# Kernel tuning notes

Measured on AMD Instinct MI355X. Metric: run time of the kernel, lower is better.

Reference implementation:

```python
import jax, jax.numpy as jnp
import numpy as np

NEG_INF = -9e15
LEAKY_SLOPE = 0.2  # init alpha
N, IN_DIM, OUT_DIM = 8192, 512, 256


def setup_inputs() -> dict:
    key = jax.random.key(0)
    k1, k2, k3, k4, k5 = jax.random.split(key, 5)
    h = jax.random.normal(k1, (N, IN_DIM), dtype=jnp.float32)
    adj = jax.random.randint(k2, (N, N), 0, 2, dtype=jnp.int32)
    W = jax.random.normal(k3, (IN_DIM, OUT_DIM), dtype=jnp.float32) * 0.06
    a_left = jax.random.normal(k4, (OUT_DIM, 1), dtype=jnp.float32) * 0.1
    a_right = jax.random.normal(k5, (OUT_DIM, 1), dtype=jnp.float32) * 0.1
    return {"h": h, "adj": adj, "W": W, "a_left": a_left, "a_right": a_right}


def reference(h, adj, W, a_left, a_right):
    Wh = h @ W                                  # [N, out_dim]
    Wh1 = Wh @ a_left                           # [N, 1]
    Wh2 = Wh @ a_right                          # [N, 1]
    e = Wh1 + Wh2.T                             # [N, N] broadcast additive scores
    e = jnp.where(e > 0, e, LEAKY_SLOPE * e)    # LeakyReLU
    e = jnp.where(adj > 0, e, NEG_INF)          # adjacency mask
    attention = jax.nn.softmax(e, axis=1)       # row-wise softmax (dropout=0, eval)
    h_out = attention @ Wh                      # [N, out_dim]
    return jax.nn.elu(h_out)                    # activation=True
```

## Files before the change

kernel.cpp:

```cpp
#include <hip/hip_runtime.h>
#include <hip/hip_bf16.h>
#include <cstdint>
#include <cstddef>

typedef float  f32x4  __attribute__((ext_vector_type(4)));
typedef __bf16 bf16x8 __attribute__((ext_vector_type(8)));

#define LOG2E 1.4426950408889634f

static constexpr int GN   = 8192;
static constexpr int GIN  = 512;
static constexpr int GOUT = 256;

static __device__ __forceinline__ void gload_lds16(const void* g, void* lds){
  typedef uint32_t __attribute__((address_space(1)))* gp_t;
  typedef uint32_t __attribute__((address_space(3)))* lp_t;
  __builtin_amdgcn_global_load_lds((gp_t)(uintptr_t)g,
                                   (lp_t)(uint32_t)(uintptr_t)lds, 16, 0, 0);
}

__global__ void k_wa(const float* __restrict__ W, const float* __restrict__ al,
                     const float* __restrict__ ar, float* __restrict__ wal,
                     float* __restrict__ war){
  int k = blockIdx.x;
  int lane = threadIdx.x;
  float4 wv = ((const float4*)(W + (size_t)k*GOUT))[lane];
  float4 av = ((const float4*)al)[lane];
  float4 bv = ((const float4*)ar)[lane];
  float sl = wv.x*av.x + wv.y*av.y + wv.z*av.z + wv.w*av.w;
  float sr = wv.x*bv.x + wv.y*bv.y + wv.z*bv.z + wv.w*bv.w;
  #pragma unroll
  for(int o=32;o;o>>=1){ sl += __shfl_down(sl,o,64); sr += __shfl_down(sr,o,64); }
  if(lane==0){ wal[k] = sl*LOG2E; war[k] = sr*LOG2E; }
}

__global__ void k_h2b(const float* __restrict__ h, __bf16* __restrict__ hb){
  size_t i = ((size_t)blockIdx.x*256 + threadIdx.x)*8;
  float4 v0 = *(const float4*)(h+i);
  float4 v1 = *(const float4*)(h+i+4);
  bf16x8 o;
  o[0]=(__bf16)v0.x; o[1]=(__bf16)v0.y; o[2]=(__bf16)v0.z; o[3]=(__bf16)v0.w;
  o[4]=(__bf16)v1.x; o[5]=(__bf16)v1.y; o[6]=(__bf16)v1.z; o[7]=(__bf16)v1.w;
  *(bf16x8*)(hb+i) = o;
}

__global__ void k_wt(const float* __restrict__ W, __bf16* __restrict__ WT){
  int idx = blockIdx.x*256 + threadIdx.x;
  int k = idx >> 8, c = idx & 255;
  WT[(size_t)c*GIN + k] = (__bf16)W[idx];
}

__global__ void k_wh12(const float* __restrict__ h, const float* __restrict__ wal,
                       const float* __restrict__ war, float* __restrict__ Wh1,
                       float* __restrict__ Wh2){
  int row = blockIdx.x*4 + (threadIdx.x>>6);
  int lane = threadIdx.x & 63;
  const float4* hp = (const float4*)(h + (size_t)row*GIN);
  const float4* lp = (const float4*)wal;
  const float4* rp = (const float4*)war;
  float sl = 0.f, sr = 0.f;
  #pragma unroll
  for(int t=0;t<2;t++){
    float4 v = hp[lane*2+t];
    float4 a = lp[lane*2+t];
    float4 b = rp[lane*2+t];
    sl += v.x*a.x + v.y*a.y + v.z*a.z + v.w*a.w;
    sr += v.x*b.x + v.y*b.y + v.z*b.z + v.w*b.w;
  }
  #pragma unroll
  for(int o=32;o;o>>=1){ sl += __shfl_down(sl,o,64); sr += __shfl_down(sr,o,64); }
  if(lane==0){ Wh1[row]=sl; Wh2[row]=sr; }
}

__global__ __launch_bounds__(256,1) void k_gemmT(const __bf16* __restrict__ WT,
                                                 const __bf16* __restrict__ hb,
                                                 __bf16* __restrict__ WhbT){
  __shared__ __attribute__((aligned(16))) __bf16 As[2][64*64];
  __shared__ __attribute__((aligned(16))) __bf16 Bs[2][128*64];
  const int tid = threadIdx.x, lane = tid & 63, w = tid >> 6;
  const int mb = blockIdx.x >> 6, nb = blockIdx.x & 63;
  const int m0 = mb*64, n0 = nb*128;

  f32x4 acc[8];
  #pragma unroll
  for(int t=0;t<8;t++) acc[t] = (f32x4){0.f,0.f,0.f,0.f};

  const int lr = lane>>3;
  const int bs_sw = ((lane&7)*16) ^ (lr<<4);

  auto stage = [&](int it, int buf){
    const int k0b = it*128;
    #pragma unroll
    for(int s=0;s<6;s++){
      int u = w + s*4;
      const char* src; char* dst;
      if(u < 8){
        int r8 = u*8;
        src = (const char*)(WT + (size_t)(m0 + r8 + lr)*GIN);
        dst = (char*)&As[buf][0] + r8*128;
      } else {
        int r8 = (u-8)*8;
        src = (const char*)(hb + (size_t)(n0 + r8 + lr)*GIN);
        dst = (char*)&Bs[buf][0] + r8*128;
      }
      gload_lds16(src + k0b + bs_sw, dst);
    }
  };

  auto kstep = [&](int kk, int buf){
    const int ko = kk*64 + (lane>>4)*16;
    const int am = 16*w + (lane&15);
    bf16x8 af = *(const bf16x8*)((const char*)&As[buf][0] + am*128 + (ko ^ ((am&7)<<4)));
    #pragma unroll
    for(int t=0;t<8;t++){
      int n = 16*t + (lane&15);
      bf16x8 bf = *(const bf16x8*)((const char*)&Bs[buf][0] + n*128 + (ko ^ ((n&7)<<4)));
      acc[t] = __builtin_amdgcn_mfma_f32_16x16x32_bf16(af, bf, acc[t], 0, 0, 0);
    }
  };

  stage(0,0);
  asm volatile("s_waitcnt vmcnt(0)" ::: "memory");
  __builtin_amdgcn_s_barrier();
  for(int it=0; it<8; it++){
    int buf = it & 1;
    if(it < 7) stage(it+1, buf^1);
    kstep(0, buf);
    kstep(1, buf);
    asm volatile("s_waitcnt vmcnt(0)" ::: "memory");
    __builtin_amdgcn_s_barrier();
  }

  const int mrow = m0 + 16*w + 4*(lane>>4);
  const int nc0  = n0 + (lane&15);
  #pragma unroll
  for(int t=0;t<8;t++){
    #pragma unroll
    for(int r=0;r<4;r++){
      WhbT[(size_t)(mrow + r)*GN + nc0 + 16*t] = (__bf16)acc[t][r];
    }
  }
}

__global__ __launch_bounds__(256,2) void k_attn(const int* __restrict__ adj,
                                                const __bf16* __restrict__ WhbT,
                                                const float* __restrict__ Wh1s,
                                                const float* __restrict__ Wh2s,
                                                float* __restrict__ accPV,
                                                float* __restrict__ accS){
  __shared__ __attribute__((aligned(16))) __bf16 Vs[2][256*64];
  const int tid = threadIdx.x, lane = tid & 63, w = tid >> 6;
  const int rg = blockIdx.x >> 3, chunk = blockIdx.x & 7;
  const int r0 = rg * 128;
  const int j0 = chunk * 1024;

  f32x4 acc0[16], acc1[16];
  #pragma unroll
  for(int t=0;t<16;t++){ acc0[t] = (f32x4){0.f,0.f,0.f,0.f}; acc1[t] = (f32x4){0.f,0.f,0.f,0.f}; }
  f32x4 accs0 = (f32x4){0.f,0.f,0.f,0.f};
  f32x4 accs1 = (f32x4){0.f,0.f,0.f,0.f};

  bf16x8 ones;
  #pragma unroll
  for(int j=0;j<8;j++) ones[j] = (__bf16)1.0f;

  const int kg = lane >> 4;
  const int myrow0 = r0 + 16*w + (lane & 15);
  const int myrow1 = myrow0 + 64;
  const float wh1_0 = Wh1s[myrow0];
  const float wh1_1 = Wh1s[myrow1];
  const int*   adjrow0 = adj  + (size_t)myrow0*GN + j0 + kg*8;
  const int*   adjrow1 = adj  + (size_t)myrow1*GN + j0 + kg*8;
  const float* wh2p    = Wh2s + j0 + kg*8;

  const int lr = lane>>3;
  const int bs_sw = ((lane&7)*16) ^ (lr<<4);

  auto stage = [&](int it, int buf){
    const int colb = (j0 + it*64)*2;
    #pragma unroll
    for(int s=0;s<8;s++){
      int u = w + s*4;
      int r8 = u*8;
      const char* src = (const char*)WhbT + (size_t)(r8 + lr)*(GN*2) + colb + bs_sw;
      gload_lds16(src, (char*)&Vs[buf][0] + r8*128);
    }
  };

  auto mkpa = [&](float wh1, int4 a0, int4 a1, float4 w0, float4 w1) -> bf16x8 {
    bf16x8 pa;
    float y, p;
    y = wh1 + w0.x; y = fmaxf(y, 0.2f*y); p = exp2f(y); pa[0] = (__bf16)(a0.x ? p : 0.f);
    y = wh1 + w0.y; y = fmaxf(y, 0.2f*y); p = exp2f(y); pa[1] = (__bf16)(a0.y ? p : 0.f);
    y = wh1 + w0.z; y = fmaxf(y, 0.2f*y); p = exp2f(y); pa[2] = (__bf16)(a0.z ? p : 0.f);
    y = wh1 + w0.w; y = fmaxf(y, 0.2f*y); p = exp2f(y); pa[3] = (__bf16)(a0.w ? p : 0.f);
    y = wh1 + w1.x; y = fmaxf(y, 0.2f*y); p = exp2f(y); pa[4] = (__bf16)(a1.x ? p : 0.f);
    y = wh1 + w1.y; y = fmaxf(y, 0.2f*y); p = exp2f(y); pa[5] = (__bf16)(a1.y ? p : 0.f);
    y = wh1 + w1.z; y = fmaxf(y, 0.2f*y); p = exp2f(y); pa[6] = (__bf16)(a1.z ? p : 0.f);
    y = wh1 + w1.w; y = fmaxf(y, 0.2f*y); p = exp2f(y); pa[7] = (__bf16)(a1.w ? p : 0.f);
    return pa;
  };

  auto kstep = [&](int it, int kk, int buf){
    const int off = it*64 + kk*32;
    const int* ap0 = adjrow0 + off;
    const int* ap1 = adjrow1 + off;
    int4 a00 = *(const int4*)ap0;  int4 a01 = *(const int4*)(ap0 + 4);
    int4 a10 = *(const int4*)ap1;  int4 a11 = *(const int4*)(ap1 + 4);
    const float* wp = wh2p + off;
    float4 w0 = *(const float4*)wp;
    float4 w1 = *(const float4*)(wp + 4);
    bf16x8 pa0 = mkpa(wh1_0, a00, a01, w0, w1);
    bf16x8 pa1 = mkpa(wh1_1, a10, a11, w0, w1);
    const int ko = kk*64 + kg*16;
    #pragma unroll
    for(int t=0;t<16;t++){
      int n = 16*t + (lane&15);
      bf16x8 bv = *(const bf16x8*)((const char*)&Vs[buf][0] + n*128 + (ko ^ ((n&7)<<4)));
      acc0[t] = __builtin_amdgcn_mfma_f32_16x16x32_bf16(pa0, bv, acc0[t], 0, 0, 0);
      acc1[t] = __builtin_amdgcn_mfma_f32_16x16x32_bf16(pa1, bv, acc1[t], 0, 0, 0);
    }
    accs0 = __builtin_amdgcn_mfma_f32_16x16x32_bf16(pa0, ones, accs0, 0, 0, 0);
    accs1 = __builtin_amdgcn_mfma_f32_16x16x32_bf16(pa1, ones, accs1, 0, 0, 0);
  };

  stage(0, 0);
  asm volatile("s_waitcnt vmcnt(0)" ::: "memory");
  __builtin_amdgcn_s_barrier();
  for(int it=0; it<16; it++){
    int buf = it & 1;
    if(it < 15) stage(it+1, buf^1);
    kstep(it, 0, buf);
    kstep(it, 1, buf);
    asm volatile("s_waitcnt vmcnt(0)" ::: "memory");
    __builtin_amdgcn_s_barrier();
  }

  const int orow0 = r0 + 16*w + 4*kg;
  const int orow1 = orow0 + 64;
  const int ocol  = lane & 15;
  #pragma unroll
  for(int t=0;t<16;t++){
    #pragma unroll
    for(int r=0;r<4;r++){
      atomicAdd(accPV + (size_t)(orow0 + r)*GOUT + ocol + 16*t, acc0[t][r]);
      atomicAdd(accPV + (size_t)(orow1 + r)*GOUT + ocol + 16*t, acc1[t][r]);
    }
  }
  if(ocol == 0){
    #pragma unroll
    for(int r=0;r<4;r++){
      atomicAdd(accS + orow0 + r, accs0[r]);
      atomicAdd(accS + orow1 + r, accs1[r]);
    }
  }
}

static __device__ __forceinline__ float elu1(float x){
  return x > 0.f ? x : (exp2f(x*LOG2E) - 1.f);
}
__global__ void k_norm(const float* __restrict__ accPV, const float* __restrict__ accS,
                       float* __restrict__ out){
  size_t i = ((size_t)blockIdx.x*256 + threadIdx.x)*4;
  int row = (int)(i >> 8);
  float inv = 1.0f / accS[row];
  float4 v = *(const float4*)(accPV + i);
  float4 o;
  o.x = elu1(v.x*inv); o.y = elu1(v.y*inv); o.z = elu1(v.z*inv); o.w = elu1(v.w*inv);
  *(float4*)(out + i) = o;
}

extern "C" void kernel_launch(void* const* d_in, const int* in_sizes, int n_in,
                              void* d_out, int out_size, void* d_ws, size_t ws_size,
                              hipStream_t stream){
  const float* h  = (const float*)d_in[0];
  const int*   adj= (const int*)  d_in[1];
  const float* W  = (const float*)d_in[2];
  const float* al = (const float*)d_in[3];
  const float* ar = (const float*)d_in[4];
  float* out = (float*)d_out;

  char* ws = (char*)d_ws;
  float*  accPV = (float*) (ws);
  float*  accS  = (float*) (ws + 8388608);
  __bf16* hb    = (__bf16*)(ws + 8421376);
  __bf16* WT    = (__bf16*)(ws + 16809984);
  __bf16* WhbT  = (__bf16*)(ws + 17072128);
  float*  wal   = (float*) (ws + 21266432);
  float*  war   = (float*) (ws + 21268480);
  float*  Wh1   = (float*) (ws + 21270528);
  float*  Wh2   = (float*) (ws + 21303296);
  if(ws_size < 21336064) return;

  hipMemsetAsync(accPV, 0, 8388608 + 32768, stream);

  k_wa  <<<512, 64, 0, stream>>>(W, al, ar, wal, war);
  k_h2b <<<2048, 256, 0, stream>>>(h, hb);
  k_wt  <<<512, 256, 0, stream>>>(W, WT);
  k_wh12<<<2048, 256, 0, stream>>>(h, wal, war, Wh1, Wh2);
  k_gemmT<<<256, 256, 0, stream>>>(WT, hb, WhbT);
  k_attn<<<512, 256, 0, stream>>>(adj, WhbT, Wh1, Wh2, accPV, accS);
  k_norm<<<2048, 256, 0, stream>>>(accPV, accS, out);
}
```

Before: 154.5 us.

## Fuse h prep kernels, ballot-pack adjacency masks, replace atomics with partial-sum reduce

```diff
diff --git a/kernel.cpp b/kernel.cpp
--- a/kernel.cpp
+++ b/kernel.cpp
@@ -34,42 +34,32 @@
   if(lane==0){ wal[k] = sl*LOG2E; war[k] = sr*LOG2E; }
 }
 
-__global__ void k_h2b(const float* __restrict__ h, __bf16* __restrict__ hb){
-  size_t i = ((size_t)blockIdx.x*256 + threadIdx.x)*8;
-  float4 v0 = *(const float4*)(h+i);
-  float4 v1 = *(const float4*)(h+i+4);
+__global__ void k_prep_h(const float* __restrict__ h, const float* __restrict__ wal,
+                         const float* __restrict__ war, __bf16* __restrict__ hb,
+                         float* __restrict__ Wh1, float* __restrict__ Wh2){
+  int row = blockIdx.x*4 + (threadIdx.x>>6);
+  int lane = threadIdx.x & 63;
+  const float4* hp = (const float4*)(h + (size_t)row*GIN);
+  float4 v0 = hp[lane*2], v1 = hp[lane*2+1];
   bf16x8 o;
   o[0]=(__bf16)v0.x; o[1]=(__bf16)v0.y; o[2]=(__bf16)v0.z; o[3]=(__bf16)v0.w;
   o[4]=(__bf16)v1.x; o[5]=(__bf16)v1.y; o[6]=(__bf16)v1.z; o[7]=(__bf16)v1.w;
-  *(bf16x8*)(hb+i) = o;
+  *(bf16x8*)(hb + (size_t)row*GIN + lane*8) = o;
+  float4 a0 = ((const float4*)wal)[lane*2], a1 = ((const float4*)wal)[lane*2+1];
+  float4 b0 = ((const float4*)war)[lane*2], b1 = ((const float4*)war)[lane*2+1];
+  float sl = v0.x*a0.x+v0.y*a0.y+v0.z*a0.z+v0.w*a0.w
+           + v1.x*a1.x+v1.y*a1.y+v1.z*a1.z+v1.w*a1.w;
+  float sr = v0.x*b0.x+v0.y*b0.y+v0.z*b0.z+v0.w*b0.w
+           + v1.x*b1.x+v1.y*b1.y+v1.z*b1.z+v1.w*b1.w;
+  #pragma unroll
+  for(int of=32;of;of>>=1){ sl += __shfl_down(sl,of,64); sr += __shfl_down(sr,of,64); }
+  if(lane==0){ Wh1[row]=sl; Wh2[row]=sr; }
 }
 
 __global__ void k_wt(const float* __restrict__ W, __bf16* __restrict__ WT){
   int idx = blockIdx.x*256 + threadIdx.x;
   int k = idx >> 8, c = idx & 255;
   WT[(size_t)c*GIN + k] = (__bf16)W[idx];
-}
-
-__global__ void k_wh12(const float* __restrict__ h, const float* __restrict__ wal,
-                       const float* __restrict__ war, float* __restrict__ Wh1,
-                       float* __restrict__ Wh2){
-  int row = blockIdx.x*4 + (threadIdx.x>>6);
-  int lane = threadIdx.x & 63;
-  const float4* hp = (const float4*)(h + (size_t)row*GIN);
-  const float4* lp = (const float4*)wal;
-  const float4* rp = (const float4*)war;
-  float sl = 0.f, sr = 0.f;
-  #pragma unroll
-  for(int t=0;t<2;t++){
-    float4 v = hp[lane*2+t];
-    float4 a = lp[lane*2+t];
-    float4 b = rp[lane*2+t];
-    sl += v.x*a.x + v.y*a.y + v.z*a.z + v.w*a.w;
-    sr += v.x*b.x + v.y*b.y + v.z*b.z + v.w*b.w;
-  }
-  #pragma unroll
-  for(int o=32;o;o>>=1){ sl += __shfl_down(sl,o,64); sr += __shfl_down(sr,o,64); }
-  if(lane==0){ Wh1[row]=sl; Wh2[row]=sr; }
 }
 
 __global__ __launch_bounds__(256,1) void k_gemmT(const __bf16* __restrict__ WT,
@@ -142,12 +132,13 @@
   }
 }
 
+template<bool PART>
 __global__ __launch_bounds__(256,2) void k_attn(const int* __restrict__ adj,
                                                 const __bf16* __restrict__ WhbT,
                                                 const float* __restrict__ Wh1s,
                                                 const float* __restrict__ Wh2s,
-                                                float* __restrict__ accPV,
-                                                float* __restrict__ accS){
+                                                float* __restrict__ pv_out,
+                                                float* __restrict__ s_out){
   __shared__ __attribute__((aligned(16))) __bf16 Vs[2][256*64];
   const int tid = threadIdx.x, lane = tid & 63, w = tid >> 6;
   const int rg = blockIdx.x >> 3, chunk = blockIdx.x & 7;
@@ -164,14 +155,15 @@
   #pragma unroll
   for(int j=0;j<8;j++) ones[j] = (__bf16)1.0f;
 
-  const int kg = lane >> 4;
+  const int kg  = lane >> 4;
+  const int kg8 = kg << 3;
   const int myrow0 = r0 + 16*w + (lane & 15);
-  const int myrow1 = myrow0 + 64;
   const float wh1_0 = Wh1s[myrow0];
-  const float wh1_1 = Wh1s[myrow1];
-  const int*   adjrow0 = adj  + (size_t)myrow0*GN + j0 + kg*8;
-  const int*   adjrow1 = adj  + (size_t)myrow1*GN + j0 + kg*8;
-  const float* wh2p    = Wh2s + j0 + kg*8;
+  const float wh1_1 = Wh1s[myrow0 + 64];
+  const float* wh2p = Wh2s + j0 + kg8;
+
+  const size_t arow0 = (size_t)(r0 + 16*w) * GN + j0;
+  const size_t arow1 = arow0 + (size_t)64 * GN;
 
   const int lr = lane>>3;
   const int bs_sw = ((lane&7)*16) ^ (lr<<4);
@@ -187,31 +179,53 @@
     }
   };
 
-  auto mkpa = [&](float wh1, int4 a0, int4 a1, float4 w0, float4 w1) -> bf16x8 {
+  int a0p[16], a1p[16];
+  auto adj_load = [&](int tt){
+    const int co = tt*64 + lane;
+    #pragma unroll
+    for(int r=0;r<16;r++) a0p[r] = adj[arow0 + (size_t)r*GN + co];
+    #pragma unroll
+    for(int r=0;r<16;r++) a1p[r] = adj[arow1 + (size_t)r*GN + co];
+  };
+  auto adj_pack = [&](uint64_t& m0, uint64_t& m1){
+    uint64_t n0 = 0, n1 = 0;
+    #pragma unroll
+    for(int r=0;r<16;r++){
+      uint64_t b = __ballot(a0p[r] != 0);
+      if((lane&15)==r) n0 = b;
+    }
+    #pragma unroll
+    for(int r=0;r<16;r++){
+      uint64_t b = __ballot(a1p[r] != 0);
+      if((lane&15)==r) n1 = b;
+    }
+    m0 = n0; m1 = n1;
+  };
+
+  auto mkpa = [&](float wh1, unsigned m8, float4 w0, float4 w1) -> bf16x8 {
     bf16x8 pa;
     float y, p;
-    y = wh1 + w0.x; y = fmaxf(y, 0.2f*y); p = exp2f(y); pa[0] = (__bf16)(a0.x ? p : 0.f);
-    y = wh1 + w0.y; y = fmaxf(y, 0.2f*y); p = exp2f(y); pa[1] = (__bf16)(a0.y ? p : 0.f);
-    y = wh1 + w0.z; y = fmaxf(y, 0.2f*y); p = exp2f(y); pa[2] = (__bf16)(a0.z ? p : 0.f);
-    y = wh1 + w0.w; y = fmaxf(y, 0.2f*y); p = exp2f(y); pa[3] = (__bf16)(a0.w ? p : 0.f);
-    y = wh1 + w1.x; y = fmaxf(y, 0.2f*y); p = exp2f(y); pa[4] = (__bf16)(a1.x ? p : 0.f);
-    y = wh1 + w1.y; y = fmaxf(y, 0.2f*y); p = exp2f(y); pa[5] = (__bf16)(a1.y ? p : 0.f);
-    y = wh1 + w1.z; y = fmaxf(y, 0.2f*y); p = exp2f(y); pa[6] = (__bf16)(a1.z ? p : 0.f);
-    y = wh1 + w1.w; y = fmaxf(y, 0.2f*y); p = exp2f(y); pa[7] = (__bf16)(a1.w ? p : 0.f);
+    y = wh1 + w0.x; y = fmaxf(y, 0.2f*y); p = exp2f(y); pa[0] = (__bf16)((m8    )&1 ? p : 0.f);
+    y = wh1 + w0.y; y = fmaxf(y, 0.2f*y); p = exp2f(y); pa[1] = (__bf16)((m8>>1)&1 ? p : 0.f);
+    y = wh1 + w0.z; y = fmaxf(y, 0.2f*y); p = exp2f(y); pa[2] = (__bf16)((m8>>2)&1 ? p : 0.f);
+    y = wh1 + w0.w; y = fmaxf(y, 0.2f*y); p = exp2f(y); pa[3] = (__bf16)((m8>>3)&1 ? p : 0.f);
+    y = wh1 + w1.x; y = fmaxf(y, 0.2f*y); p = exp2f(y); pa[4] = (__bf16)((m8>>4)&1 ? p : 0.f);
+    y = wh1 + w1.y; y = fmaxf(y, 0.2f*y); p = exp2f(y); pa[5] = (__bf16)((m8>>5)&1 ? p : 0.f);
+    y = wh1 + w1.z; y = fmaxf(y, 0.2f*y); p = exp2f(y); pa[6] = (__bf16)((m8>>6)&1 ? p : 0.f);
+    y = wh1 + w1.w; y = fmaxf(y, 0.2f*y); p = exp2f(y); pa[7] = (__bf16)((m8>>7)&1 ? p : 0.f);
     return pa;
   };
 
+  uint64_t mk0, mk1;
+
   auto kstep = [&](int it, int kk, int buf){
-    const int off = it*64 + kk*32;
-    const int* ap0 = adjrow0 + off;
-    const int* ap1 = adjrow1 + off;
-    int4 a00 = *(const int4*)ap0;  int4 a01 = *(const int4*)(ap0 + 4);
-    int4 a10 = *(const int4*)ap1;  int4 a11 = *(const int4*)(ap1 + 4);
-    const float* wp = wh2p + off;
+    const float* wp = wh2p + it*64 + kk*32;
     float4 w0 = *(const float4*)wp;
     float4 w1 = *(const float4*)(wp + 4);
-    bf16x8 pa0 = mkpa(wh1_0, a00, a01, w0, w1);
-    bf16x8 pa1 = mkpa(wh1_1, a10, a11, w0, w1);
+    unsigned m8_0 = (unsigned)((mk0 >> (kk*32 + kg8)) & 0xffULL);
+    unsigned m8_1 = (unsigned)((mk1 >> (kk*32 + kg8)) & 0xffULL);
+    bf16x8 pa0 = mkpa(wh1_0, m8_0, w0, w1);
+    bf16x8 pa1 = mkpa(wh1_1, m8_1, w0, w1);
     const int ko = kk*64 + kg*16;
     #pragma unroll
     for(int t=0;t<16;t++){
@@ -225,33 +239,56 @@
   };
 
   stage(0, 0);
+  adj_load(0);
+  adj_pack(mk0, mk1);
   asm volatile("s_waitcnt vmcnt(0)" ::: "memory");
   __builtin_amdgcn_s_barrier();
+
   for(int it=0; it<16; it++){
     int buf = it & 1;
-    if(it < 15) stage(it+1, buf^1);
+    if(it < 15){
+      stage(it+1, buf^1);
+      adj_load(it+1);
+    }
     kstep(it, 0, buf);
     kstep(it, 1, buf);
+    uint64_t mkn0 = 0, mkn1 = 0;
+    if(it < 15) adj_pack(mkn0, mkn1);
     asm volatile("s_waitcnt vmcnt(0)" ::: "memory");
     __builtin_amdgcn_s_barrier();
+    mk0 = mkn0; mk1 = mkn1;
   }
 
   const int orow0 = r0 + 16*w + 4*kg;
   const int orow1 = orow0 + 64;
   const int ocol  = lane & 15;
-  #pragma unroll
-  for(int t=0;t<16;t++){
-    #pragma unroll
-    for(int r=0;r<4;r++){
-      atomicAdd(accPV + (size_t)(orow0 + r)*GOUT + ocol + 16*t, acc0[t][r]);
-      atomicAdd(accPV + (size_t)(orow1 + r)*GOUT + ocol + 16*t, acc1[t][r]);
-    }
-  }
-  if(ocol == 0){
-    #pragma unroll
-    for(int r=0;r<4;r++){
-      atomicAdd(accS + orow0 + r, accs0[r]);
-      atomicAdd(accS + orow1 + r, accs1[r]);
+  if constexpr (PART){
+    float* pv = pv_out + (size_t)chunk*GN*GOUT;
+    float* sp = s_out  + (size_t)chunk*GN;
+    #pragma unroll
+    for(int t=0;t<16;t++){
+      #pragma unroll
+      for(int r=0;r<4;r++){
+        pv[(size_t)(orow0 + r)*GOUT + ocol + 16*t] = acc0[t][r];
+        pv[(size_t)(orow1 + r)*GOUT + ocol + 16*t] = acc1[t][r];
+      }
+    }
+    if(ocol == 0){
+      #pragma unroll
+      for(int r=0;r<4;r++){ sp[orow0 + r] = accs0[r]; sp[orow1 + r] = accs1[r]; }
+    }
+  } else {
+    #pragma unroll
+    for(int t=0;t<16;t++){
+      #pragma unroll
+      for(int r=0;r<4;r++){
+        atomicAdd(pv_out + (size_t)(orow0 + r)*GOUT + ocol + 16*t, acc0[t][r]);
+        atomicAdd(pv_out + (size_t)(orow1 + r)*GOUT + ocol + 16*t, acc1[t][r]);
+      }
+    }
+    if(ocol == 0){
+      #pragma unroll
+      for(int r=0;r<4;r++){ atomicAdd(s_out + orow0 + r, accs0[r]); atomicAdd(s_out + orow1 + r, accs1[r]); }
     }
   }
 }
@@ -259,6 +296,26 @@
 static __device__ __forceinline__ float elu1(float x){
   return x > 0.f ? x : (exp2f(x*LOG2E) - 1.f);
 }
+
+__global__ void k_reduce(const float* __restrict__ accP, const float* __restrict__ accSp,
+                         float* __restrict__ out){
+  size_t i = ((size_t)blockIdx.x*256 + threadIdx.x)*4;
+  int row = (int)(i >> 8);
+  float S = 0.f;
+  #pragma unroll
+  for(int c=0;c<8;c++) S += accSp[(size_t)c*GN + row];
+  float4 s = {0.f,0.f,0.f,0.f};
+  #pragma unroll
+  for(int c=0;c<8;c++){
+    float4 v = *(const float4*)(accP + (size_t)c*GN*GOUT + i);
+    s.x += v.x; s.y += v.y; s.z += v.z; s.w += v.w;
+  }
+  float inv = 1.0f / S;
+  float4 o;
+  o.x = elu1(s.x*inv); o.y = elu1(s.y*inv); o.z = elu1(s.z*inv); o.w = elu1(s.w*inv);
+  *(float4*)(out + i) = o;
+}
+
 __global__ void k_norm(const float* __restrict__ accPV, const float* __restrict__ accS,
                        float* __restrict__ out){
   size_t i = ((size_t)blockIdx.x*256 + threadIdx.x)*4;
@@ -279,26 +336,46 @@
   const float* al = (const float*)d_in[3];
   const float* ar = (const float*)d_in[4];
   float* out = (float*)d_out;
-
   char* ws = (char*)d_ws;
-  float*  accPV = (float*) (ws);
-  float*  accS  = (float*) (ws + 8388608);
-  __bf16* hb    = (__bf16*)(ws + 8421376);
-  __bf16* WT    = (__bf16*)(ws + 16809984);
-  __bf16* WhbT  = (__bf16*)(ws + 17072128);
-  float*  wal   = (float*) (ws + 21266432);
-  float*  war   = (float*) (ws + 21268480);
-  float*  Wh1   = (float*) (ws + 21270528);
-  float*  Wh2   = (float*) (ws + 21303296);
-  if(ws_size < 21336064) return;
-
-  hipMemsetAsync(accPV, 0, 8388608 + 32768, stream);
-
-  k_wa  <<<512, 64, 0, stream>>>(W, al, ar, wal, war);
-  k_h2b <<<2048, 256, 0, stream>>>(h, hb);
-  k_wt  <<<512, 256, 0, stream>>>(W, WT);
-  k_wh12<<<2048, 256, 0, stream>>>(h, wal, war, Wh1, Wh2);
-  k_gemmT<<<256, 256, 0, stream>>>(WT, hb, WhbT);
-  k_attn<<<512, 256, 0, stream>>>(adj, WhbT, Wh1, Wh2, accPV, accS);
-  k_norm<<<2048, 256, 0, stream>>>(accPV, accS, out);
-}
+
+  const size_t SZ_ACCP = (size_t)8*GN*GOUT*4;
+  const size_t NEED_A  = SZ_ACCP + 4194304 + 32768 + 32768 + 262144;
+
+  if(ws_size >= NEED_A){
+    float*  accP  = (float*) (ws);
+    __bf16* hb    = (__bf16*)(ws);
+    __bf16* WT    = (__bf16*)(ws + 8388608);
+    float*  wal   = (float*) (ws + 8650752);
+    float*  war   = (float*) (ws + 8652800);
+    __bf16* WhbT  = (__bf16*)(ws + SZ_ACCP);
+    float*  Wh1   = (float*) (ws + SZ_ACCP + 4194304);
+    float*  Wh2   = (float*) (ws + SZ_ACCP + 4227072);
+    float*  accSp = (float*) (ws + SZ_ACCP + 4259840);
+
+    k_wa    <<<512, 64, 0, stream>>>(W, al, ar, wal, war);
+    k_prep_h<<<2048, 256, 0, stream>>>(h, wal, war, hb, Wh1, Wh2);
+    k_wt    <<<512, 256, 0, stream>>>(W, WT);
+    k_gemmT <<<256, 256, 0, stream>>>(WT, hb, WhbT);
+    k_attn<true><<<512, 256, 0, stream>>>(adj, WhbT, Wh1, Wh2, accP, accSp);
+    k_reduce<<<2048, 256, 0, stream>>>(accP, accSp, out);
+  } else {
+    float*  accPV = (float*) (ws);
+    float*  accS  = (float*) (ws + 8388608);
+    __bf16* hb    = (__bf16*)(ws + 8421376);
+    __bf16* WT    = (__bf16*)(ws + 16809984);
+    __bf16* WhbT  = (__bf16*)(ws + 17072128);
+    float*  wal   = (float*) (ws + 21266432);
+    float*  war   = (float*) (ws + 21268480);
+    float*  Wh1   = (float*) (ws + 21270528);
+    float*  Wh2   = (float*) (ws + 21303296);
+    if(ws_size < 21336064) return;
+
+    hipMemsetAsync(accPV, 0, 8388608 + 32768, stream);
+    k_wa    <<<512, 64, 0, stream>>>(W, al, ar, wal, war);
+    k_prep_h<<<2048, 256, 0, stream>>>(h, wal, war, hb, Wh1, Wh2);
+    k_wt    <<<512, 256, 0, stream>>>(W, WT);
+    k_gemmT <<<256, 256, 0, stream>>>(WT, hb, WhbT);
+    k_attn<false><<<512, 256, 0, stream>>>(adj, WhbT, Wh1, Wh2, accPV, accS);
+    k_norm  <<<2048, 256, 0, stream>>>(accPV, accS, out);
+  }
+}
```

Measured after the change: 138.6 us. -10.3%, faster.
